# Performance work log

Measured on AMD Instinct MI355X. Metric: run time of the kernel, lower is better.

Reference implementation:

```python
import jax, jax.numpy as jnp
import numpy as np

N_HEAD = 16
D_HEAD = 64
D_MODEL = 1024
D_INNER = 4096
QLEN = 1024
MLEN = 1024
BSZ = 2
LN_EPS = 1e-5


def _layer_norm(x, g, b, eps=LN_EPS):
    mu = jnp.mean(x, axis=-1, keepdims=True)
    var = jnp.var(x, axis=-1, keepdims=True)
    return (x - mu) * jax.lax.rsqrt(var + eps) * g + b


def _rel_shift(x):
    # x: [qlen, rlen, bsz, n_head]
    q, r, b, n = x.shape
    zp = jnp.zeros((q, 1, b, n), x.dtype)
    xp = jnp.concatenate([zp, x], axis=1).reshape(r + 1, q, b, n)
    return xp[1:].reshape(q, r, b, n)


def setup_inputs() -> dict:
    key = jax.random.key(0)
    ks = jax.random.split(key, 12)
    klen = MLEN + QLEN
    w = jax.random.normal(ks[0], (QLEN, BSZ, D_MODEL), jnp.float32)
    r = jax.random.normal(ks[1], (klen, D_MODEL), jnp.float32)
    mems = jax.random.normal(ks[2], (MLEN, BSZ, D_MODEL), jnp.float32)
    # causal mask: query i attends keys j <= i + mlen
    i = jnp.arange(QLEN)[:, None]
    j = jnp.arange(klen)[None, :]
    attn_mask = (j > i + MLEN)[:, :, None]  # [qlen, klen, 1] bool
    s = 0.02
    params = dict(
        qkv_w=jax.random.normal(ks[3], (3 * N_HEAD * D_HEAD, D_MODEL), jnp.float32) * s,
        r_net_w=jax.random.normal(ks[4], (N_HEAD * D_HEAD, D_MODEL), jnp.float32) * s,
        o_w=jax.random.normal(ks[5], (D_MODEL, N_HEAD * D_HEAD), jnp.float32) * s,
        r_r_bias=jax.random.normal(ks[6], (N_HEAD, D_HEAD), jnp.float32) * s,
        r_w_bias=jax.random.normal(ks[7], (N_HEAD, D_HEAD), jnp.float32) * s,
        ln1_g=jnp.ones((D_MODEL,), jnp.float32),
        ln1_b=jnp.zeros((D_MODEL,), jnp.float32),
        ff_w1=jax.random.normal(ks[8], (D_INNER, D_MODEL), jnp.float32) * s,
        ff_b1=jnp.zeros((D_INNER,), jnp.float32),
        ff_w2=jax.random.normal(ks[9], (D_MODEL, D_INNER), jnp.float32) * s,
        ff_b2=jnp.zeros((D_MODEL,), jnp.float32),
        ln2_g=jnp.ones((D_MODEL,), jnp.float32),
        ln2_b=jnp.zeros((D_MODEL,), jnp.float32),
    )
    return dict(w=w, r=r, mems=mems, attn_mask=attn_mask, **params)


def reference(w, r, mems, attn_mask, qkv_w, r_net_w, o_w, r_r_bias, r_w_bias,
              ln1_g, ln1_b, ff_w1, ff_b1, ff_w2, ff_b2, ln2_g, ln2_b):
    qlen, bsz = w.shape[0], w.shape[1]
    scale = 1.0 / (D_HEAD ** 0.5)
    cat = jnp.concatenate([mems, w], axis=0)              # [klen, b, d_model]
    klen = cat.shape[0]
    w_heads = cat @ qkv_w.T                                # [klen, b, 3*n*d]
    wq, wk, wv = jnp.split(w_heads, 3, axis=-1)
    wq = wq[-qlen:]
    r_head_k = (r @ r_net_w.T).reshape(-1, N_HEAD, D_HEAD)  # [rlen, n, d]
    wq = wq.reshape(qlen, bsz, N_HEAD, D_HEAD)
    wk = wk.reshape(klen, bsz, N_HEAD, D_HEAD)
    wv = wv.reshape(klen, bsz, N_HEAD, D_HEAD)
    AC = jnp.einsum('ibnd,jbnd->ijbn', wq + r_w_bias, wk)   # content term
    BD = jnp.einsum('ibnd,jnd->ijbn', wq + r_r_bias, r_head_k)
    BD = _rel_shift(BD)                                     # position term
    attn_score = (AC + BD) * scale
    mask_value = jnp.finfo(attn_score.dtype).min
    attn_score = jnp.where(attn_mask[:, :, :, None], mask_value, attn_score)
    attn_prob = jax.nn.softmax(attn_score, axis=1)
    attn_vec = jnp.einsum('ijbn,jbnd->ibnd', attn_prob, wv)
    attn_vec = attn_vec.reshape(qlen, bsz, N_HEAD * D_HEAD)
    attn_out = attn_vec @ o_w.T
    h = _layer_norm(w + attn_out, ln1_g, ln1_b)             # post-lnorm
    core = jax.nn.relu(h @ ff_w1.T + ff_b1) @ ff_w2.T + ff_b2
    out = _layer_norm(h + core, ln2_g, ln2_b)
    return out
```

## Files before the change

### kernel.cpp

```cpp
#include <hip/hip_runtime.h>
#include <math.h>

#define QLEN 1024
#define MLEN 1024
#define KLEN 2048
#define BSZc 2
#define NH 16
#define DH 64
#define DM 1024
#define DI 4096

typedef unsigned short ushort_t;
typedef __attribute__((ext_vector_type(8))) short short8;
typedef __attribute__((ext_vector_type(4))) float f32x4;

__device__ __forceinline__ ushort_t f2bf(float x) {
    unsigned int u = __float_as_uint(x);
    unsigned int r = (u + 0x7FFFu + ((u >> 16) & 1u)) >> 16;
    return (ushort_t)r;
}

__device__ __forceinline__ void gload_lds16(const ushort_t* g, ushort_t* l) {
    __builtin_amdgcn_global_load_lds(
        (const __attribute__((address_space(1))) unsigned int*)g,
        (__attribute__((address_space(3))) unsigned int*)l,
        16, 0, 0);
}

__device__ __forceinline__ void cast8(const float* s, ushort_t* d, int g) {
    const float4 a = *(const float4*)(s + g * 8);
    const float4 b = *(const float4*)(s + g * 8 + 4);
    short8 o;
    o[0] = (short)f2bf(a.x); o[1] = (short)f2bf(a.y);
    o[2] = (short)f2bf(a.z); o[3] = (short)f2bf(a.w);
    o[4] = (short)f2bf(b.x); o[5] = (short)f2bf(b.y);
    o[6] = (short)f2bf(b.z); o[7] = (short)f2bf(b.w);
    *(short8*)(d + g * 8) = o;
}

__global__ __launch_bounds__(256)
void cast_phase1(const float* __restrict__ qkv_w, const float* __restrict__ rnet_w,
                 const float* __restrict__ mems, const float* __restrict__ w,
                 const float* __restrict__ r,
                 ushort_t* __restrict__ W1, ushort_t* __restrict__ W2,
                 ushort_t* __restrict__ Acat, ushort_t* __restrict__ Rsrc)
{
    int g = blockIdx.x * 256 + threadIdx.x;
    if (g < 393216)            { cast8(qkv_w,  W1,              g); }
    else if (g < 524288)       { cast8(rnet_w, W2,              g - 393216); }
    else if (g < 786432)       { cast8(mems,   Acat,            g - 524288); }
    else if (g < 1048576)      { cast8(w,      Acat + 2097152,  g - 786432); }
    else if (g < 1310720)      { cast8(r,      Rsrc,            g - 1048576); }
}

__global__ __launch_bounds__(256)
void cast_phase2(const float* __restrict__ o_w, const float* __restrict__ ffw1,
                 const float* __restrict__ ffw2,
                 ushort_t* __restrict__ W3, ushort_t* __restrict__ W4,
                 ushort_t* __restrict__ W5)
{
    int g = blockIdx.x * 256 + threadIdx.x;
    if (g < 131072)            { cast8(o_w,  W3, g); }
    else if (g < 655360)       { cast8(ffw1, W4, g - 131072); }
    else if (g < 1179648)      { cast8(ffw2, W5, g - 655360); }
}

template<int EMODE, int ACT, int BN, int SPLIT>
__global__ __launch_bounds__(256)
void gemm_mfma(const ushort_t* __restrict__ A, const ushort_t* __restrict__ B,
               const float* __restrict__ bias,
               void* __restrict__ O0v, void* __restrict__ O1v,
               int M, int N, int Ks, int lda, int ldb)
{
    constexpr int JT = BN / 32;
    __shared__ ushort_t At0[128 * 32];
    __shared__ ushort_t At1[128 * 32];
    __shared__ ushort_t Bt0[BN * 32];
    __shared__ ushort_t Bt1[BN * 32];

    const int tid  = threadIdx.x;
    const int lane = tid & 63;
    const int w    = tid >> 6;
    const int lr   = lane & 15;
    const int quad = lane >> 4;
    const int m0   = blockIdx.x * 128;
    const int n0   = blockIdx.y * BN;
    const int z    = (SPLIT > 1) ? (int)blockIdx.z : 0;
    const int kbase = z * Ks;
    const int wm0  = (w >> 1) * 64;
    const int wn0  = (w & 1) * (BN / 2);

    f32x4 acc[4][JT];
#pragma unroll
    for (int it = 0; it < 4; ++it)
#pragma unroll
        for (int jt = 0; jt < JT; ++jt) acc[it][jt] = (f32x4){0.f, 0.f, 0.f, 0.f};

    const int srow = lane >> 2;
    const int scol = (lane & 3) << 3;
    const ushort_t* Ag = A + (size_t)(m0 + w * 32 + srow) * lda + kbase + scol;
    ushort_t* a00 = At0 + (w * 32) * 32;
    ushort_t* a01 = At0 + (w * 32 + 16) * 32;
    ushort_t* a10 = At1 + (w * 32) * 32;
    ushort_t* a11 = At1 + (w * 32 + 16) * 32;
    const ushort_t* Bg;
    ushort_t *b00, *b01 = nullptr, *b10, *b11 = nullptr;
    if (BN == 128) {
        Bg  = B + (size_t)(n0 + w * 32 + srow) * ldb + kbase + scol;
        b00 = Bt0 + (w * 32) * 32;
        b01 = Bt0 + (w * 32 + 16) * 32;
        b10 = Bt1 + (w * 32) * 32;
        b11 = Bt1 + (w * 32 + 16) * 32;
    } else {
        Bg  = B + (size_t)(n0 + w * 16 + srow) * ldb + kbase + scol;
        b00 = Bt0 + (w * 16) * 32;
        b10 = Bt1 + (w * 16) * 32;
    }

    const ushort_t* Ato0 = At0 + (wm0 + lr) * 32 + quad * 8;
    const ushort_t* Ato1 = At1 + (wm0 + lr) * 32 + quad * 8;
    const ushort_t* Bto0 = Bt0 + (wn0 + lr) * 32 + quad * 8;
    const ushort_t* Bto1 = Bt1 + (wn0 + lr) * 32 + quad * 8;

    for (int k0 = 0; k0 < Ks; k0 += 64) {
        __syncthreads();
        gload_lds16(Ag + k0, a00);
        gload_lds16(Ag + (size_t)16 * lda + k0, a01);
        gload_lds16(Ag + k0 + 32, a10);
        gload_lds16(Ag + (size_t)16 * lda + k0 + 32, a11);
        if (BN == 128) {
            gload_lds16(Bg + k0, b00);
            gload_lds16(Bg + (size_t)16 * ldb + k0, b01);
            gload_lds16(Bg + k0 + 32, b10);
            gload_lds16(Bg + (size_t)16 * ldb + k0 + 32, b11);
        } else {
            gload_lds16(Bg + k0, b00);
            gload_lds16(Bg + k0 + 32, b10);
        }
        __syncthreads();

        short8 af[4], bf[JT];
#pragma unroll
        for (int it = 0; it < 4; ++it)
            af[it] = *(const short8*)(Ato0 + it * 16 * 32);
#pragma unroll
        for (int jt = 0; jt < JT; ++jt)
            bf[jt] = *(const short8*)(Bto0 + jt * 16 * 32);
#pragma unroll
        for (int it = 0; it < 4; ++it)
#pragma unroll
            for (int jt = 0; jt < JT; ++jt)
                acc[it][jt] = __builtin_amdgcn_mfma_f32_16x16x32_bf16(
                    af[it], bf[jt], acc[it][jt], 0, 0, 0);
#pragma unroll
        for (int it = 0; it < 4; ++it)
            af[it] = *(const short8*)(Ato1 + it * 16 * 32);
#pragma unroll
        for (int jt = 0; jt < JT; ++jt)
            bf[jt] = *(const short8*)(Bto1 + jt * 16 * 32);
#pragma unroll
        for (int it = 0; it < 4; ++it)
#pragma unroll
            for (int jt = 0; jt < JT; ++jt)
                acc[it][jt] = __builtin_amdgcn_mfma_f32_16x16x32_bf16(
                    af[it], bf[jt], acc[it][jt], 0, 0, 0);
    }

#pragma unroll
    for (int it = 0; it < 4; ++it)
#pragma unroll
        for (int jt = 0; jt < JT; ++jt)
#pragma unroll
            for (int rg = 0; rg < 4; ++rg) {
                const int m = m0 + wm0 + it * 16 + quad * 4 + rg;
                const int n = n0 + wn0 + jt * 16 + lr;
                float v = acc[it][jt][rg];
                if (EMODE == 0) {
                    float* dst = (float*)(z ? O1v : O0v);
                    if (bias && z == 0) v += bias[n];
                    dst[(size_t)m * N + n] = v;
                } else {
                    v += bias[n];
                    if (ACT == 1) v = fmaxf(v, 0.f);
                    ((ushort_t*)O0v)[(size_t)m * N + n] = f2bf(v);
                }
            }
}

__global__ __launch_bounds__(256)
void gemm_qkvr(const ushort_t* __restrict__ Acat, const ushort_t* __restrict__ W1,
               const ushort_t* __restrict__ Rsrc, const ushort_t* __restrict__ W2,
               ushort_t* __restrict__ Qac, ushort_t* __restrict__ Qbd,
               ushort_t* __restrict__ Kbf, ushort_t* __restrict__ Vtb,
               ushort_t* __restrict__ Rh,
               const float* __restrict__ rwb, const float* __restrict__ rrb)
{
    __shared__ ushort_t At[128 * 32];
    __shared__ ushort_t Bt[128 * 32];

    const int bid  = blockIdx.x;
    const bool isr = bid >= 768;
    const ushort_t* A; const ushort_t* B; int m0, n0;
    if (!isr) { A = Acat; B = W1; m0 = (bid & 31) * 128; n0 = (bid >> 5) * 128; }
    else { int t = bid - 768; A = Rsrc; B = W2; m0 = (t & 15) * 128; n0 = (t >> 4) * 128; }
    const int K = 1024;

    const int tid  = threadIdx.x;
    const int lane = tid & 63;
    const int w    = tid >> 6;
    const int lr   = lane & 15;
    const int quad = lane >> 4;
    const int wm0  = (w >> 1) * 64;
    const int wn0  = (w & 1) * 64;

    f32x4 acc[4][4];
#pragma unroll
    for (int it = 0; it < 4; ++it)
#pragma unroll
        for (int jt = 0; jt < 4; ++jt) acc[it][jt] = (f32x4){0.f, 0.f, 0.f, 0.f};

    const int srow = lane >> 2;
    const int scol = (lane & 3) << 3;
    const ushort_t* Ag = A + (size_t)(m0 + w * 32 + srow) * K + scol;
    const ushort_t* Bg = B + (size_t)(n0 + w * 32 + srow) * K + scol;
    ushort_t* lA0 = At + (w * 32) * 32;
    ushort_t* lA1 = At + (w * 32 + 16) * 32;
    ushort_t* lB0 = Bt + (w * 32) * 32;
    ushort_t* lB1 = Bt + (w * 32 + 16) * 32;

    const ushort_t* Ato = At + (wm0 + lr) * 32 + quad * 8;
    const ushort_t* Bto = Bt + (wn0 + lr) * 32 + quad * 8;

    for (int k0 = 0; k0 < K; k0 += 32) {
        __syncthreads();
        gload_lds16(Ag + k0, lA0);
        gload_lds16(Ag + (size_t)16 * K + k0, lA1);
        gload_lds16(Bg + k0, lB0);
        gload_lds16(Bg + (size_t)16 * K + k0, lB1);
        __syncthreads();

        short8 af[4], bf[4];
#pragma unroll
        for (int it = 0; it < 4; ++it)
            af[it] = *(const short8*)(Ato + it * 16 * 32);
#pragma unroll
        for (int jt = 0; jt < 4; ++jt)
            bf[jt] = *(const short8*)(Bto + jt * 16 * 32);
#pragma unroll
        for (int it = 0; it < 4; ++it)
#pragma unroll
            for (int jt = 0; jt < 4; ++jt)
                acc[it][jt] = __builtin_amdgcn_mfma_f32_16x16x32_bf16(
                    af[it], bf[jt], acc[it][jt], 0, 0, 0);
    }

#pragma unroll
    for (int it = 0; it < 4; ++it)
#pragma unroll
        for (int jt = 0; jt < 4; ++jt)
#pragma unroll
            for (int rg = 0; rg < 4; ++rg) {
                const int m = m0 + wm0 + it * 16 + quad * 4 + rg;
                const int n = n0 + wn0 + jt * 16 + lr;
                const float v = acc[it][jt][rg];
                if (!isr) {
                    const int j = m >> 1, b = m & 1;
                    const int part = n >> 10, hh = (n >> 6) & 15, d = n & 63;
                    if (part == 0) {
                        if (j >= MLEN) {
                            const int qi = j - MLEN;
                            const size_t qidx = (((size_t)(b * NH + hh)) * QLEN + qi) * DH + d;
                            Qac[qidx] = f2bf(v + rwb[hh * DH + d]);
                            Qbd[qidx] = f2bf(v + rrb[hh * DH + d]);
                        }
                    } else if (part == 1) {
                        Kbf[(((size_t)(b * NH + hh)) * KLEN + j) * DH + d] = f2bf(v);
                    } else {
                        Vtb[(((size_t)(b * NH + hh)) * DH + d) * KLEN + j] = f2bf(v);
                    }
                } else {
                    const int hh = n >> 6, d = n & 63;
                    Rh[(((size_t)hh) * KLEN + m) * DH + d] = f2bf(v);
                }
            }
}

__global__ __launch_bounds__(256, 3)
void attn_mfma(const ushort_t* __restrict__ Qac, const ushort_t* __restrict__ Qbd,
               const ushort_t* __restrict__ Kb, const ushort_t* __restrict__ Vt,
               const ushort_t* __restrict__ Rb,
               float* __restrict__ Op0, float* __restrict__ Op1,
               float* __restrict__ Mp, float* __restrict__ Lp)
{
    __shared__ __align__(16) ushort_t Kt[64 * 72];
    __shared__ __align__(16) ushort_t Rt[128 * 72];
    __shared__ __align__(16) float    Bw[4][16][84];
    ushort_t* Vl = (ushort_t*)&Bw[0][0][0];

    const int tid  = threadIdx.x;
    const int lane = tid & 63;
    const int w    = tid >> 6;
    const int lr   = lane & 15;
    const int quad = lane >> 4;
    const int qt   = blockIdx.x;
    const int s    = blockIdx.y;
    const int bh   = blockIdx.z;
    const int i0   = qt << 6;
    const int h    = bh & 15;
    const int b    = bh >> 4;

    short8 qaf[2], qbf[2];
    {
        const size_t rowoff = ((size_t)bh * QLEN + i0 + w * 16 + lr) * DH;
#pragma unroll
        for (int kt = 0; kt < 2; ++kt) {
            qaf[kt] = *(const short8*)(Qac + rowoff + kt * 32 + quad * 8);
            qbf[kt] = *(const short8*)(Qbd + rowoff + kt * 32 + quad * 8);
        }
    }

    f32x4 O[4];
#pragma unroll
    for (int nt = 0; nt < 4; ++nt) O[nt] = (f32x4){0.f, 0.f, 0.f, 0.f};
    float m_run = -3.4e38f, l_run = 0.f;

    const int nc   = qt + 17;
    const int half = (nc + 1) >> 1;
    const int c_lo = s ? half : 0;
    const int c_hi = s ? nc : half;
    const int stw  = 3 - w;
    const float SC = 0.125f * 1.44269504f;
    const ushort_t* Kh  = Kb + (size_t)bh * KLEN * DH;
    const ushort_t* Vh  = Vt + (size_t)bh * DH * KLEN;
    const ushort_t* Rhp = Rb + (size_t)h * KLEN * DH;

    for (int c = c_lo; c < c_hi; ++c) {
        const int j0 = c << 6;
        const int wb = 960 - i0 + j0;

#pragma unroll
        for (int t = 0; t < 2; ++t) {
            int f = tid + (t << 8);
            int row = f >> 3, c8 = (f & 7) << 3;
            *(int4*)&Kt[row * 72 + c8] = *(const int4*)(Kh + (size_t)(j0 + row) * DH + c8);
        }
        if (c == c_lo) {
#pragma unroll
            for (int t = 0; t < 4; ++t) {
                int f = tid + (t << 8);
                int rl2 = f >> 3, c8 = (f & 7) << 3;
                int g = wb + rl2;
                int gc = g > (KLEN - 1) ? (KLEN - 1) : g;
                *(int4*)&Rt[((g) & 127) * 72 + c8] = *(const int4*)(Rhp + (size_t)gc * DH + c8);
            }
        } else {
#pragma unroll
            for (int t = 0; t < 2; ++t) {
                int f = tid + (t << 8);
                int rl2 = (f >> 3) + 64, c8 = (f & 7) << 3;
                int g = wb + rl2;
                int gc = g > (KLEN - 1) ? (KLEN - 1) : g;
                *(int4*)&Rt[((g) & 127) * 72 + c8] = *(const int4*)(Rhp + (size_t)gc * DH + c8);
            }
        }
        __syncthreads();

#pragma unroll
        for (int ctl = 0; ctl < 5; ++ctl) {
            const int wr = (stw + ctl) * 16 + lr;
            const int ring = (wb + wr) & 127;
            f32x4 z = (f32x4){0.f, 0.f, 0.f, 0.f};
#pragma unroll
            for (int kt = 0; kt < 2; ++kt) {
                short8 rb2 = *(const short8*)&Rt[ring * 72 + kt * 32 + quad * 8];
                z = __builtin_amdgcn_mfma_f32_16x16x32_bf16(qbf[kt], rb2, z, 0, 0, 0);
            }
#pragma unroll
            for (int rg = 0; rg < 4; ++rg)
                Bw[w][quad * 4 + rg][ctl * 16 + lr] = z[rg];
        }
#pragma unroll
        for (int ct = 0; ct < 4; ++ct) {
            f32x4 z = (f32x4){0.f, 0.f, 0.f, 0.f};
#pragma unroll
            for (int kt = 0; kt < 2; ++kt) {
                short8 kb2 = *(const short8*)&Kt[(ct * 16 + lr) * 72 + kt * 32 + quad * 8];
                z = __builtin_amdgcn_mfma_f32_16x16x32_bf16(qaf[kt], kb2, z, 0, 0, 0);
            }
#pragma unroll
            for (int rg = 0; rg < 4; ++rg) {
                const int rrow = quad * 4 + rg;
                Bw[w][rrow][ct * 16 + lr + 15 - rrow] += z[rg];
            }
        }

        const int lim = i0 + w * 16 + lr + 1024 - j0;
        float pv[16];
        float mx = -3.4e38f;
#pragma unroll
        for (int kt = 0; kt < 2; ++kt)
#pragma unroll
            for (int t = 0; t < 8; ++t) {
                const int jj = kt * 32 + quad * 8 + t;
                float sv = Bw[w][lr][jj + 15 - lr] * SC;
                sv = (jj > lim) ? -3.4e38f : sv;
                pv[kt * 8 + t] = sv;
                mx = fmaxf(mx, sv);
            }
        mx = fmaxf(mx, __shfl_xor(mx, 16, 64));
        mx = fmaxf(mx, __shfl_xor(mx, 32, 64));
        const float m_new = fmaxf(m_run, mx);
        float ps = 0.f;
        short8 pf[2];
#pragma unroll
        for (int kt = 0; kt < 2; ++kt)
#pragma unroll
            for (int t = 0; t < 8; ++t) {
                const float e = exp2f(pv[kt * 8 + t] - m_new);
                ps += e;
                pf[kt][t] = (short)f2bf(e);
            }
        ps += __shfl_xor(ps, 16, 64);
        ps += __shfl_xor(ps, 32, 64);
        const float alpha = exp2f(m_run - m_new);
        m_run = m_new;
        l_run = l_run * alpha + ps;

        __syncthreads();

#pragma unroll
        for (int t = 0; t < 2; ++t) {
            int f = tid + (t << 8);
            int d = f >> 3, c8 = (f & 7) << 3;
            *(int4*)&Vl[d * 72 + c8] = *(const int4*)(Vh + (size_t)d * KLEN + j0 + c8);
        }
        __syncthreads();

        float ar[4];
#pragma unroll
        for (int rg = 0; rg < 4; ++rg)
            ar[rg] = __shfl(alpha, quad * 4 + rg, 64);
#pragma unroll
        for (int nt = 0; nt < 4; ++nt) {
            O[nt][0] *= ar[0]; O[nt][1] *= ar[1];
            O[nt][2] *= ar[2]; O[nt][3] *= ar[3];
        }
#pragma unroll
        for (int kt = 0; kt < 2; ++kt)
#pragma unroll
            for (int nt = 0; nt < 4; ++nt) {
                short8 vb = *(const short8*)&Vl[(nt * 16 + lr) * 72 + kt * 32 + quad * 8];
                O[nt] = __builtin_amdgcn_mfma_f32_16x16x32_bf16(pf[kt], vb, O[nt], 0, 0, 0);
            }
    }

    if (quad == 0) {
        const size_t mi = ((size_t)s * 32 + bh) * QLEN + i0 + w * 16 + lr;
        Mp[mi] = m_run;
        Lp[mi] = l_run;
    }
    float* Op = s ? Op1 : Op0;
#pragma unroll
    for (int nt = 0; nt < 4; ++nt)
#pragma unroll
        for (int rg = 0; rg < 4; ++rg) {
            const int i = i0 + w * 16 + quad * 4 + rg;
            Op[((size_t)i * BSZc + b) * DM + h * DH + nt * 16 + lr] = O[nt][rg];
        }
}

__global__ __launch_bounds__(256)
void attn_merge(const float* __restrict__ O0, const float* __restrict__ O1,
                const float* __restrict__ Mp, const float* __restrict__ Lp,
                ushort_t* __restrict__ AV)
{
    const int row = blockIdx.x;
    const int tid = threadIdx.x;
    const int i = row >> 1, b = row & 1;
    const int h = tid >> 4;
    const int bh = b * NH + h;
    const size_t mi = (size_t)bh * QLEN + i;
    const float m1 = Mp[mi],             l1 = Lp[mi];
    const float m2 = Mp[32 * QLEN + mi], l2 = Lp[32 * QLEN + mi];
    const float M = fmaxf(m1, m2);
    const float a1 = exp2f(m1 - M), a2 = exp2f(m2 - M);
    const float rl = 1.f / (l1 * a1 + l2 * a2);
    const float f1 = a1 * rl, f2 = a2 * rl;
    const float4 o1 = ((const float4*)(O0 + (size_t)row * DM))[tid];
    const float4 o2 = ((const float4*)(O1 + (size_t)row * DM))[tid];
    ushort_t* p = AV + (size_t)row * DM + tid * 4;
    p[0] = f2bf(o1.x * f1 + o2.x * f2);
    p[1] = f2bf(o1.y * f1 + o2.y * f2);
    p[2] = f2bf(o1.z * f1 + o2.z * f2);
    p[3] = f2bf(o1.w * f1 + o2.w * f2);
}

__global__ __launch_bounds__(256)
void add_ln(const float* __restrict__ X, const float* __restrict__ Y0,
            const float* __restrict__ Y1,
            const float* __restrict__ gg, const float* __restrict__ bb,
            float* __restrict__ out, ushort_t* __restrict__ outb)
{
    const int row  = blockIdx.x;
    const int tid  = threadIdx.x;
    const int lane = tid & 63;
    const int w    = tid >> 6;
    __shared__ float ssum[4], ssq[4];

    const float4 xv = ((const float4*)(X + (size_t)row * DM))[tid];
    const float4 yv = ((const float4*)(Y0 + (size_t)row * DM))[tid];
    float v0 = xv.x + yv.x, v1 = xv.y + yv.y;
    float v2 = xv.z + yv.z, v3 = xv.w + yv.w;
    if (Y1) {
        const float4 zv = ((const float4*)(Y1 + (size_t)row * DM))[tid];
        v0 += zv.x; v1 += zv.y; v2 += zv.z; v3 += zv.w;
    }
    float s = v0 + v1 + v2 + v3;
    float q = v0 * v0 + v1 * v1 + v2 * v2 + v3 * v3;
#pragma unroll
    for (int off = 32; off > 0; off >>= 1) {
        s += __shfl_xor(s, off, 64);
        q += __shfl_xor(q, off, 64);
    }
    if (lane == 0) { ssum[w] = s; ssq[w] = q; }
    __syncthreads();
    s = ssum[0] + ssum[1] + ssum[2] + ssum[3];
    q = ssq[0] + ssq[1] + ssq[2] + ssq[3];
    const float mean = s * (1.f / DM);
    const float var  = q * (1.f / DM) - mean * mean;
    const float rs   = rsqrtf(var + 1e-5f);
    const float4 g4 = ((const float4*)gg)[tid];
    const float4 b4 = ((const float4*)bb)[tid];
    float4 ov;
    ov.x = (v0 - mean) * rs * g4.x + b4.x;
    ov.y = (v1 - mean) * rs * g4.y + b4.y;
    ov.z = (v2 - mean) * rs * g4.z + b4.z;
    ov.w = (v3 - mean) * rs * g4.w + b4.w;
    ((float4*)(out + (size_t)row * DM))[tid] = ov;
    if (outb) {
        ushort_t* p = outb + (size_t)row * DM + tid * 4;
        p[0] = f2bf(ov.x); p[1] = f2bf(ov.y);
        p[2] = f2bf(ov.z); p[3] = f2bf(ov.w);
    }
}

extern "C" void kernel_launch(void* const* d_in, const int* in_sizes, int n_in,
                              void* d_out, int out_size, void* d_ws, size_t ws_size,
                              hipStream_t stream)
{
    (void)in_sizes; (void)n_in; (void)out_size; (void)ws_size;
    const float* w      = (const float*)d_in[0];
    const float* r      = (const float*)d_in[1];
    const float* mems   = (const float*)d_in[2];
    const float* qkv_w  = (const float*)d_in[4];
    const float* rnet_w = (const float*)d_in[5];
    const float* o_w    = (const float*)d_in[6];
    const float* r_r_b  = (const float*)d_in[7];
    const float* r_w_b  = (const float*)d_in[8];
    const float* ln1g   = (const float*)d_in[9];
    const float* ln1b   = (const float*)d_in[10];
    const float* ffw1   = (const float*)d_in[11];
    const float* ffb1   = (const float*)d_in[12];
    const float* ffw2   = (const float*)d_in[13];
    const float* ffb2   = (const float*)d_in[14];
    const float* ln2g   = (const float*)d_in[15];
    const float* ln2b   = (const float*)d_in[16];
    float* out = (float*)d_out;

    char* wsb = (char*)d_ws;
    const size_t MB = 1024 * 1024;
    ushort_t* W1    = (ushort_t*)(wsb + 0 * MB);
    ushort_t* W2    = (ushort_t*)(wsb + 6 * MB);
    ushort_t* Acat  = (ushort_t*)(wsb + 8 * MB);
    ushort_t* Rsrc  = (ushort_t*)(wsb + 16 * MB);
    ushort_t* Qac   = (ushort_t*)(wsb + 20 * MB);
    ushort_t* Qbd   = (ushort_t*)(wsb + 24 * MB);
    ushort_t* Kbf   = (ushort_t*)(wsb + 28 * MB);
    ushort_t* Vt    = (ushort_t*)(wsb + 36 * MB);
    ushort_t* Rh    = (ushort_t*)(wsb + 44 * MB);
    float*    Op0   = (float*)(wsb + 48 * MB);
    float*    Op1   = (float*)(wsb + 56 * MB);
    float*    Mp    = (float*)(wsb + 4 * MB);
    float*    Lp    = (float*)(wsb + 4 * MB + 512 * 1024);
    ushort_t* AVec  = (ushort_t*)(wsb + 0 * MB);
    ushort_t* W3    = (ushort_t*)(wsb + 4 * MB);
    float*    AOut0 = (float*)(wsb + 8 * MB);
    float*    AOut1 = (float*)(wsb + 44 * MB);
    float*    Hbuf  = (float*)(wsb + 16 * MB);
    ushort_t* Hbf   = (ushort_t*)(wsb + 24 * MB);
    ushort_t* W4    = (ushort_t*)(wsb + 28 * MB);
    ushort_t* FFbf  = (ushort_t*)(wsb + 36 * MB);
    ushort_t* W5    = (ushort_t*)(wsb + 52 * MB);
    float*    Core0 = (float*)(wsb + 0 * MB);
    float*    Core1 = (float*)(wsb + 8 * MB);

    dim3 blk(256);

    cast_phase1<<<dim3(5120), blk, 0, stream>>>(qkv_w, rnet_w, mems, w, r,
                                                W1, W2, Acat, Rsrc);

    gemm_qkvr<<<dim3(896), blk, 0, stream>>>(
        Acat, W1, Rsrc, W2, Qac, Qbd, Kbf, Vt, Rh, r_w_b, r_r_b);

    attn_mfma<<<dim3(16, 2, 32), blk, 0, stream>>>(
        Qac, Qbd, Kbf, Vt, Rh, Op0, Op1, Mp, Lp);

    attn_merge<<<dim3(2048), blk, 0, stream>>>(Op0, Op1, Mp, Lp, AVec);

    cast_phase2<<<dim3(4608), blk, 0, stream>>>(o_w, ffw1, ffw2, W3, W4, W5);

    gemm_mfma<0, 0, 64, 2><<<dim3(16, 16, 2), blk, 0, stream>>>(
        AVec, W3, nullptr, AOut0, AOut1, 2048, 1024, 512, 1024, 1024);

    add_ln<<<dim3(2 * QLEN), blk, 0, stream>>>(w, AOut0, AOut1, ln1g, ln1b, Hbuf, Hbf);

    gemm_mfma<3, 1, 128, 1><<<dim3(16, 32), blk, 0, stream>>>(
        Hbf, W4, ffb1, FFbf, nullptr, 2048, 4096, 1024, 1024, 1024);

    gemm_mfma<0, 0, 64, 2><<<dim3(16, 16, 2), blk, 0, stream>>>(
        FFbf, W5, ffb2, Core0, Core1, 2048, 1024, 2048, 4096, 4096);

    add_ln<<<dim3(2 * QLEN), blk, 0, stream>>>(Hbuf, Core0, Core1, ln2g, ln2b, out, nullptr);
}
```

Baseline: 398.2 us.

## Register-prefetch next K/R tiles and load V fragments directly from global

The attention kernel now prefetches the next chunk's K and R rows into registers during the current iteration and writes them to LDS at loop start, overlapping global latency with compute. V fragments are read straight from global memory into MFMA operand registers instead of being staged through LDS, which removes one LDS store pass and one barrier per chunk. In exchange register pressure rises (kpf, rpf, vpf arrays) under a 3-waves launch bound, and the V global reads are less coalesced and rely on cache reuse across waves.

```diff
diff --git a/kernel.cpp b/kernel.cpp
--- a/kernel.cpp
+++ b/kernel.cpp
@@ -295,7 +295,6 @@
     __shared__ __align__(16) ushort_t Kt[64 * 72];
     __shared__ __align__(16) ushort_t Rt[128 * 72];
     __shared__ __align__(16) float    Bw[4][16][84];
-    ushort_t* Vl = (ushort_t*)&Bw[0][0][0];
 
     const int tid  = threadIdx.x;
     const int lane = tid & 63;
@@ -334,35 +333,64 @@
     const ushort_t* Vh  = Vt + (size_t)bh * DH * KLEN;
     const ushort_t* Rhp = Rb + (size_t)h * KLEN * DH;
 
+    const int srow = tid >> 3;
+    const int scol = (tid & 7) << 3;
+
+    int4 kpf[2], rpf[4];
+    {
+        const int j0 = c_lo << 6;
+        kpf[0] = *(const int4*)(Kh + (size_t)(j0 + srow) * DH + scol);
+        kpf[1] = *(const int4*)(Kh + (size_t)(j0 + srow + 32) * DH + scol);
+        const int wb = 960 - i0 + j0;
+#pragma unroll
+        for (int t = 0; t < 4; ++t) {
+            int g = wb + srow + t * 32;
+            int gc = g > (KLEN - 1) ? (KLEN - 1) : g;
+            rpf[t] = *(const int4*)(Rhp + (size_t)gc * DH + scol);
+        }
+    }
+
     for (int c = c_lo; c < c_hi; ++c) {
         const int j0 = c << 6;
         const int wb = 960 - i0 + j0;
 
-#pragma unroll
-        for (int t = 0; t < 2; ++t) {
-            int f = tid + (t << 8);
-            int row = f >> 3, c8 = (f & 7) << 3;
-            *(int4*)&Kt[row * 72 + c8] = *(const int4*)(Kh + (size_t)(j0 + row) * DH + c8);
-        }
+        *(int4*)&Kt[(size_t)srow * 72 + scol]        = kpf[0];
+        *(int4*)&Kt[(size_t)(srow + 32) * 72 + scol] = kpf[1];
         if (c == c_lo) {
 #pragma unroll
             for (int t = 0; t < 4; ++t) {
-                int f = tid + (t << 8);
-                int rl2 = f >> 3, c8 = (f & 7) << 3;
-                int g = wb + rl2;
+                int g = wb + srow + t * 32;
+                *(int4*)&Rt[(size_t)(g & 127) * 72 + scol] = rpf[t];
+            }
+        } else {
+#pragma unroll
+            for (int t = 0; t < 2; ++t) {
+                int g = wb + 64 + srow + t * 32;
+                *(int4*)&Rt[(size_t)(g & 127) * 72 + scol] = rpf[t];
+            }
+        }
+
+        short8 vpf[2][4];
+#pragma unroll
+        for (int kt = 0; kt < 2; ++kt)
+#pragma unroll
+            for (int nt = 0; nt < 4; ++nt)
+                vpf[kt][nt] = *(const short8*)(
+                    Vh + (size_t)(nt * 16 + lr) * KLEN + j0 + kt * 32 + quad * 8);
+
+        if (c + 1 < c_hi) {
+            const int j1 = j0 + 64;
+            kpf[0] = *(const int4*)(Kh + (size_t)(j1 + srow) * DH + scol);
+            kpf[1] = *(const int4*)(Kh + (size_t)(j1 + srow + 32) * DH + scol);
+            const int wb1 = wb + 64;
+#pragma unroll
+            for (int t = 0; t < 2; ++t) {
+                int g = wb1 + 64 + srow + t * 32;
                 int gc = g > (KLEN - 1) ? (KLEN - 1) : g;
-                *(int4*)&Rt[((g) & 127) * 72 + c8] = *(const int4*)(Rhp + (size_t)gc * DH + c8);
-            }
-        } else {
-#pragma unroll
-            for (int t = 0; t < 2; ++t) {
-                int f = tid + (t << 8);
-                int rl2 = (f >> 3) + 64, c8 = (f & 7) << 3;
-                int g = wb + rl2;
-                int gc = g > (KLEN - 1) ? (KLEN - 1) : g;
-                *(int4*)&Rt[((g) & 127) * 72 + c8] = *(const int4*)(Rhp + (size_t)gc * DH + c8);
-            }
-        }
+                rpf[t] = *(const int4*)(Rhp + (size_t)gc * DH + scol);
+            }
+        }
+
         __syncthreads();
 
 #pragma unroll
@@ -428,14 +456,6 @@
 
         __syncthreads();
 
-#pragma unroll
-        for (int t = 0; t < 2; ++t) {
-            int f = tid + (t << 8);
-            int d = f >> 3, c8 = (f & 7) << 3;
-            *(int4*)&Vl[d * 72 + c8] = *(const int4*)(Vh + (size_t)d * KLEN + j0 + c8);
-        }
-        __syncthreads();
-
         float ar[4];
 #pragma unroll
         for (int rg = 0; rg < 4; ++rg)
@@ -448,10 +468,8 @@
 #pragma unroll
         for (int kt = 0; kt < 2; ++kt)
 #pragma unroll
-            for (int nt = 0; nt < 4; ++nt) {
-                short8 vb = *(const short8*)&Vl[(nt * 16 + lr) * 72 + kt * 32 + quad * 8];
-                O[nt] = __builtin_amdgcn_mfma_f32_16x16x32_bf16(pf[kt], vb, O[nt], 0, 0, 0);
-            }
+            for (int nt = 0; nt < 4; ++nt)
+                O[nt] = __builtin_amdgcn_mfma_f32_16x16x32_bf16(pf[kt], vpf[kt][nt], O[nt], 0, 0, 0);
     }
 
     if (quad == 0) {
```

Result: slower. 452.8 us (+13.7%).

## Stream K/R/V tiles into XOR-swizzled LDS via direct global-to-LDS loads with prefetch

Applied to the files above, without the earlier changes.

Replaces the register-staged K, R and V tile loads in the attention kernel with global_load_lds direct-to-LDS copies. It uses an unpadded 64-wide layout with an XOR swizzle to avoid bank conflicts. The next chunk's K and R tiles are prefetched while the current chunk finishes softmax and PV, and V gets its own buffer instead of aliasing Bw, which removes one barrier per iteration. This costs more LDS per block, which may reduce occupancy under launch_bounds(256,3). The hazard ordering between the async loads and the barriers is also subtle.

```diff
diff --git a/kernel.cpp b/kernel.cpp
--- a/kernel.cpp
+++ b/kernel.cpp
@@ -292,10 +292,10 @@
                float* __restrict__ Op0, float* __restrict__ Op1,
                float* __restrict__ Mp, float* __restrict__ Lp)
 {
-    __shared__ __align__(16) ushort_t Kt[64 * 72];
-    __shared__ __align__(16) ushort_t Rt[128 * 72];
+    __shared__ __align__(16) ushort_t Kt[64 * 64];
+    __shared__ __align__(16) ushort_t Rt[128 * 64];
+    __shared__ __align__(16) ushort_t Vl[64 * 64];
     __shared__ __align__(16) float    Bw[4][16][84];
-    ushort_t* Vl = (ushort_t*)&Bw[0][0][0];
 
     const int tid  = threadIdx.x;
     const int lane = tid & 63;
@@ -334,47 +334,54 @@
     const ushort_t* Vh  = Vt + (size_t)bh * DH * KLEN;
     const ushort_t* Rhp = Rb + (size_t)h * KLEN * DH;
 
+    const int lrow = lane >> 3;
+    const int lsg  = lane & 7;
+    const int sgo  = (lsg ^ lrow) << 3;
+    const int xq   = lr & 7;
+    const int fo0  = ((quad ^ xq)) << 3;
+    const int fo1  = (((4 | quad) ^ xq)) << 3;
+
+    {
+        const int j0 = c_lo << 6;
+        const int wb = 960 - i0 + j0;
+#pragma unroll
+        for (int t = 0; t < 2; ++t) {
+            const int rb  = t * 32 + w * 8;
+            gload_lds16(Kh + (size_t)(j0 + rb + lrow) * DH + sgo,
+                        Kt + rb * 64);
+        }
+#pragma unroll
+        for (int t = 0; t < 4; ++t) {
+            const int gb = wb + t * 32 + w * 8;
+            const int g  = gb + lrow;
+            const int gc = g > (KLEN - 1) ? (KLEN - 1) : g;
+            gload_lds16(Rhp + (size_t)gc * DH + sgo,
+                        Rt + (gb & 127) * 64);
+        }
+    }
+
     for (int c = c_lo; c < c_hi; ++c) {
         const int j0 = c << 6;
         const int wb = 960 - i0 + j0;
 
+        __syncthreads();
+
 #pragma unroll
         for (int t = 0; t < 2; ++t) {
-            int f = tid + (t << 8);
-            int row = f >> 3, c8 = (f & 7) << 3;
-            *(int4*)&Kt[row * 72 + c8] = *(const int4*)(Kh + (size_t)(j0 + row) * DH + c8);
-        }
-        if (c == c_lo) {
-#pragma unroll
-            for (int t = 0; t < 4; ++t) {
-                int f = tid + (t << 8);
-                int rl2 = f >> 3, c8 = (f & 7) << 3;
-                int g = wb + rl2;
-                int gc = g > (KLEN - 1) ? (KLEN - 1) : g;
-                *(int4*)&Rt[((g) & 127) * 72 + c8] = *(const int4*)(Rhp + (size_t)gc * DH + c8);
-            }
-        } else {
-#pragma unroll
-            for (int t = 0; t < 2; ++t) {
-                int f = tid + (t << 8);
-                int rl2 = (f >> 3) + 64, c8 = (f & 7) << 3;
-                int g = wb + rl2;
-                int gc = g > (KLEN - 1) ? (KLEN - 1) : g;
-                *(int4*)&Rt[((g) & 127) * 72 + c8] = *(const int4*)(Rhp + (size_t)gc * DH + c8);
-            }
-        }
-        __syncthreads();
+            const int db = t * 32 + w * 8;
+            gload_lds16(Vh + (size_t)(db + lrow) * KLEN + j0 + sgo,
+                        Vl + db * 64);
+        }
 
 #pragma unroll
         for (int ctl = 0; ctl < 5; ++ctl) {
             const int wr = (stw + ctl) * 16 + lr;
             const int ring = (wb + wr) & 127;
             f32x4 z = (f32x4){0.f, 0.f, 0.f, 0.f};
-#pragma unroll
-            for (int kt = 0; kt < 2; ++kt) {
-                short8 rb2 = *(const short8*)&Rt[ring * 72 + kt * 32 + quad * 8];
-                z = __builtin_amdgcn_mfma_f32_16x16x32_bf16(qbf[kt], rb2, z, 0, 0, 0);
-            }
+            short8 r0 = *(const short8*)&Rt[ring * 64 + fo0];
+            z = __builtin_amdgcn_mfma_f32_16x16x32_bf16(qbf[0], r0, z, 0, 0, 0);
+            short8 r1 = *(const short8*)&Rt[ring * 64 + fo1];
+            z = __builtin_amdgcn_mfma_f32_16x16x32_bf16(qbf[1], r1, z, 0, 0, 0);
 #pragma unroll
             for (int rg = 0; rg < 4; ++rg)
                 Bw[w][quad * 4 + rg][ctl * 16 + lr] = z[rg];
@@ -382,11 +389,10 @@
 #pragma unroll
         for (int ct = 0; ct < 4; ++ct) {
             f32x4 z = (f32x4){0.f, 0.f, 0.f, 0.f};
-#pragma unroll
-            for (int kt = 0; kt < 2; ++kt) {
-                short8 kb2 = *(const short8*)&Kt[(ct * 16 + lr) * 72 + kt * 32 + quad * 8];
-                z = __builtin_amdgcn_mfma_f32_16x16x32_bf16(qaf[kt], kb2, z, 0, 0, 0);
-            }
+            short8 k0f = *(const short8*)&Kt[(ct * 16 + lr) * 64 + fo0];
+            z = __builtin_amdgcn_mfma_f32_16x16x32_bf16(qaf[0], k0f, z, 0, 0, 0);
+            short8 k1f = *(const short8*)&Kt[(ct * 16 + lr) * 64 + fo1];
+            z = __builtin_amdgcn_mfma_f32_16x16x32_bf16(qaf[1], k1f, z, 0, 0, 0);
 #pragma unroll
             for (int rg = 0; rg < 4; ++rg) {
                 const int rrow = quad * 4 + rg;
@@ -428,13 +434,23 @@
 
         __syncthreads();
 
-#pragma unroll
-        for (int t = 0; t < 2; ++t) {
-            int f = tid + (t << 8);
-            int d = f >> 3, c8 = (f & 7) << 3;
-            *(int4*)&Vl[d * 72 + c8] = *(const int4*)(Vh + (size_t)d * KLEN + j0 + c8);
-        }
-        __syncthreads();
+        if (c + 1 < c_hi) {
+            const int j1 = j0 + 64;
+#pragma unroll
+            for (int t = 0; t < 2; ++t) {
+                const int rb = t * 32 + w * 8;
+                gload_lds16(Kh + (size_t)(j1 + rb + lrow) * DH + sgo,
+                            Kt + rb * 64);
+            }
+#pragma unroll
+            for (int t = 0; t < 2; ++t) {
+                const int gb = wb + 128 + t * 32 + w * 8;
+                const int g  = gb + lrow;
+                const int gc = g > (KLEN - 1) ? (KLEN - 1) : g;
+                gload_lds16(Rhp + (size_t)gc * DH + sgo,
+                            Rt + (gb & 127) * 64);
+            }
+        }
 
         float ar[4];
 #pragma unroll
@@ -445,13 +461,19 @@
             O[nt][0] *= ar[0]; O[nt][1] *= ar[1];
             O[nt][2] *= ar[2]; O[nt][3] *= ar[3];
         }
-#pragma unroll
-        for (int kt = 0; kt < 2; ++kt)
+        {
+            short8 vb;
 #pragma unroll
             for (int nt = 0; nt < 4; ++nt) {
-                short8 vb = *(const short8*)&Vl[(nt * 16 + lr) * 72 + kt * 32 + quad * 8];
-                O[nt] = __builtin_amdgcn_mfma_f32_16x16x32_bf16(pf[kt], vb, O[nt], 0, 0, 0);
-            }
+                vb = *(const short8*)&Vl[(nt * 16 + lr) * 64 + fo0];
+                O[nt] = __builtin_amdgcn_mfma_f32_16x16x32_bf16(pf[0], vb, O[nt], 0, 0, 0);
+            }
+#pragma unroll
+            for (int nt = 0; nt < 4; ++nt) {
+                vb = *(const short8*)&Vl[(nt * 16 + lr) * 64 + fo1];
+                O[nt] = __builtin_amdgcn_mfma_f32_16x16x32_bf16(pf[1], vb, O[nt], 0, 0, 0);
+            }
+        }
     }
 
     if (quad == 0) {
```

Measured after the change: 394.0 us. No clear change (-1.1%).
